# Optimization experiments

Measured on AMD Instinct MI355X. Metric: run time of the kernel, lower is better.

The kernel has to match this reference:

```python
import jax, jax.numpy as jnp
import numpy as np

# LIF params (from norse LIFParameters in __init__)
DT = 0.001
TAU_SYN_INV = 100.0   # 1/0.01
TAU_MEM_INV = 50.0    # 1/0.02
V_TH = 0.5
V_LEAK = 0.0
V_RESET = 0.0
ALPHA = 100.0         # superspike surrogate slope
# STDP params (additive, hardbound=False)
A_PRE = 0.001
A_POST = 0.001
TAU_PRE_INV = 0.5
TAU_POST_INV = 0.5
ETA_PLUS = 0.01
ETA_MINUS = 0.0001

T_STEPS, BATCH, IN_DIM, HID, N_LBL = 50, 256, 1024, 4096, 10

@jax.custom_vjp
def spike(x):
    return (x >= 0).astype(x.dtype)

def _spike_fwd(x):
    return (x >= 0).astype(x.dtype), x

def _spike_bwd(res, g):
    # norse 'super' (SuperSpike) surrogate gradient
    return (g / (ALPHA * jnp.abs(res) + 1.0) ** 2,)

spike.defvjp(_spike_fwd, _spike_bwd)


def setup_inputs() -> dict:
    key = jax.random.key(0)
    k1, k2, k3, k4 = jax.random.split(key, 4)
    x = (jax.random.uniform(k1, (T_STEPS, BATCH, IN_DIM)) < 0.1).astype(jnp.float32)
    label = jax.random.randint(k2, (BATCH,), 0, N_LBL)
    # positive weights inside the STDP bound [0, 0.3]
    w_in0 = jax.random.uniform(k3, (HID, IN_DIM), dtype=jnp.float32) * 0.3
    w_rec0 = jax.random.uniform(k4, (HID, HID), dtype=jnp.float32) * 0.05
    return {"x": x, "label": label, "w_in0": w_in0, "w_rec0": w_rec0, "num_labels": N_LBL}


def reference(x, label, w_in0, w_rec0, num_labels):
    T, B, I = x.shape
    H = w_in0.shape[0]
    f32 = x.dtype
    # fixed block assignments (init_assignments)
    npd = H // num_labels
    assignments = jnp.clip(jnp.arange(H) // npd, 0, num_labels - 1)
    a = jax.nn.one_hot(assignments, num_labels, dtype=f32)       # (H, L)
    b = jnp.clip(a.sum(axis=0), 1.0, None)                        # (L,)

    def step(carry, pre):
        v, i, z, w_in, w_rec, tp_i, tq_i, tp_r, tq_r, sc = carry
        # --- LIF recurrent cell (norse lif_step semantics) ---
        in_cur = pre @ w_in.T + z @ w_rec.T                       # (B, H)
        v_dec = v + DT * TAU_MEM_INV * ((V_LEAK - v) + i)
        i_dec = i - DT * TAU_SYN_INV * i
        z_new = spike(v_dec - V_TH)
        v_new = (1.0 - z_new) * v_dec + z_new * V_RESET
        i_new = i_dec + in_cur
        # --- STDP on input weights (additive, no hardbound) ---
        tp_i = tp_i + DT * TAU_PRE_INV * (-tp_i + A_PRE * pre)    # (B, I) pre trace
        tq_i = tq_i + DT * TAU_POST_INV * (-tq_i + A_POST * z_new)  # (B, H) post trace
        w_in = (w_in
                + ETA_PLUS * jnp.einsum('bh,bi->hi', z_new, tp_i)
                - ETA_MINUS * jnp.einsum('bh,bi->hi', tq_i, pre))
        # --- STDP on recurrent weights; pre spikes = previous outputs (z) ---
        tp_r = tp_r + DT * TAU_PRE_INV * (-tp_r + A_PRE * z)
        tq_r = tq_r + DT * TAU_POST_INV * (-tq_r + A_POST * z_new)
        w_rec = (w_rec
                 + ETA_PLUS * jnp.einsum('bh,bj->hj', z_new, tp_r)
                 - ETA_MINUS * jnp.einsum('bh,bj->hj', tq_r, z))
        sc = sc + z_new
        return (v_new, i_new, z_new, w_in, w_rec, tp_i, tq_i, tp_r, tq_r, sc), z_new.sum()

    carry0 = (jnp.zeros((B, H), f32), jnp.zeros((B, H), f32), jnp.zeros((B, H), f32),
              w_in0, w_rec0,
              jnp.zeros((B, I), f32), jnp.zeros((B, H), f32),
              jnp.zeros((B, H), f32), jnp.zeros((B, H), f32),
              jnp.zeros((B, H), f32))
    carry, per_t = jax.lax.scan(step, carry0, x)
    _, _, _, w_in_f, w_rec_f, _, _, _, _, sc = carry
    logits = (sc @ a) / (T * b)                                   # (B, L)
    total_spikes = per_t.sum()
    spike_count = jax.ops.segment_sum(sc, label, num_segments=num_labels)  # (L, H)
    label_count = T * jax.ops.segment_sum(jnp.ones((B,), f32), label, num_segments=num_labels)
    return logits, total_spikes, w_in_f, w_rec_f, spike_count, label_count
```

## Files before the change

### kernel.cpp

```cpp
#include <hip/hip_runtime.h>

typedef unsigned short u16;
typedef unsigned char u8;
typedef unsigned int u32;
typedef long i64;
typedef __attribute__((ext_vector_type(4))) float f32x4;
typedef __attribute__((ext_vector_type(4))) int i32x4;
typedef __attribute__((ext_vector_type(4))) u16 u16x4;

#define TSTEPS 50
#define BB 256
#define II 1024
#define HH 4096
#define LL 10
#define NPLANE ((size_t)BB*HH)
#define HB ((size_t)HH*BB)
#define IB ((size_t)II*BB)
#define TC 10
#define NSLOT 11
#define QSCALE 5.0e6f
#define WSCALE 64.0f

__device__ __forceinline__ u16 f2bf(float f){
  u32 u = __float_as_uint(f);
  u += 0x7fffu + ((u >> 16) & 1u);
  return (u16)(u >> 16);
}
__device__ __forceinline__ float bf2f(u16 u){ return __uint_as_float(((u32)u) << 16); }
__device__ __forceinline__ int wrapslot(int s){ return s >= NSLOT ? s - NSLOT : s; }

__device__ __forceinline__ u8 f2fp8(float v){
  if (v < 0.0009765625f) return 0;
  if (v < 0.015625f) return (u8)__float2int_rn(v * 512.f);
  u32 b = __float_as_uint(v);
  b += 0x7ffffu + ((b >> 20) & 1u);
  int e = (int)((b >> 23) & 255) - 120;
  u32 m = (b >> 20) & 7u;
  return (u8)((e << 3) | m);
}

__device__ __forceinline__ void async_cp16(const void* g, void* l){
  auto gp = (const __attribute__((address_space(1))) void*)(unsigned long long)(g);
  auto lp = (__attribute__((address_space(3))) void*)(unsigned int)(unsigned long long)(l);
  __builtin_amdgcn_global_load_lds(gp, lp, 16, 0, 0);
}

__global__ void __launch_bounds__(256) gemm_fwd(
    const u8* __restrict__ xbt, const u8* __restrict__ wib,
    const u8* __restrict__ zb,  const u8* __restrict__ wrb,
    u16* __restrict__ pbuf)
{
  __shared__ u8 lsA[2][64*64];
  __shared__ u8 lsB[2][128*64];
  const int tid = threadIdx.x, lane = tid & 63, wid = tid >> 6;
  const int wm = wid & 1, wn = wid >> 1;

  int bid = blockIdx.x;
  int oid = (bid & 7)*80 + (bid >> 3);
  int z   = oid >> 7;
  int rem = oid & 127;
  int n0  = (rem >> 2) * 128;
  int m0  = (rem & 3) * 64;

  const u8* __restrict__ Ab; const u8* __restrict__ Bb;
  int lda, ldb, kbase;
  if (z == 0){ Ab = xbt; lda = II; Bb = wib; ldb = II; kbase = 0; }
  else       { Ab = zb;  lda = HH; Bb = wrb; ldb = HH; kbase = (z-1)*1024; }
  u16* __restrict__ C = pbuf + (size_t)z*NPLANE;

  const int lrow = lane >> 2;
  const int lcb  = (lane & 3) << 4;

  auto STAGE = [&](int buf, int k0){
    int kg = kbase + k0;
    {
      int q = wid;
      int row = q*16 + lrow;
      int cb = lcb ^ (((row >> 1) & 3) << 4);
      async_cp16(Ab + (size_t)(m0 + row)*lda + kg + cb, (char*)lsA[buf] + q*1024);
    }
#pragma unroll
    for (int c = 0; c < 2; ++c){
      int q = c*4 + wid;
      int row = q*16 + lrow;
      int cb = lcb ^ (((row >> 1) & 3) << 4);
      async_cp16(Bb + (size_t)(n0 + row)*ldb + kg + cb, (char*)lsB[buf] + q*1024);
    }
  };

  f32x4 acc[2][4];
#pragma unroll
  for (int a=0;a<2;++a)
#pragma unroll
    for (int b=0;b<4;++b) acc[a][b] = f32x4{0.f,0.f,0.f,0.f};

  const int g16 = lane >> 4;
  STAGE(0, 0);
#pragma unroll 1
  for (int kt = 0; kt < 16; ++kt){
    int cur = kt & 1;
    if (kt < 15){
      STAGE(cur ^ 1, (kt+1)*64);
      asm volatile("s_waitcnt vmcnt(3)" ::: "memory");
    } else {
      asm volatile("s_waitcnt vmcnt(0)" ::: "memory");
    }
    __builtin_amdgcn_s_barrier();
#pragma unroll
    for (int kk = 0; kk < 2; ++kk){
      int unit = kk*2 + (g16 >> 1);
      int lo8  = (g16 & 1) << 3;
      i64 af[2], bfr[4];
#pragma unroll
      for (int fm=0; fm<2; ++fm){
        int ra = wm*32 + fm*16 + (lane & 15);
        af[fm] = *(const i64*)((const char*)lsA[cur] + ra*64 +
                               (((unit ^ ((ra >> 1) & 3)) << 4) + lo8));
      }
#pragma unroll
      for (int fn=0; fn<4; ++fn){
        int rb = wn*64 + fn*16 + (lane & 15);
        bfr[fn] = *(const i64*)((const char*)lsB[cur] + rb*64 +
                                (((unit ^ ((rb >> 1) & 3)) << 4) + lo8));
      }
#pragma unroll
      for (int fm=0; fm<2; ++fm)
#pragma unroll
        for (int fn=0; fn<4; ++fn)
          acc[fm][fn] = __builtin_amdgcn_mfma_f32_16x16x32_fp8_fp8(af[fm], bfr[fn], acc[fm][fn], 0, 0, 0);
    }
    __builtin_amdgcn_s_barrier();
  }

#pragma unroll
  for (int fm=0; fm<2; ++fm)
#pragma unroll
    for (int fn=0; fn<4; ++fn)
#pragma unroll
      for (int r=0; r<4; ++r){
        int row = m0 + wm*32 + fm*16 + ((lane >> 4) << 2) + r;
        int col = n0 + wn*64 + fn*16 + (lane & 15);
        C[(size_t)row*HH + col] = f2bf(acc[fm][fn][r]);
      }
}

__global__ void __launch_bounds__(512) gemm_chunk(
    const u8* __restrict__ zRing, const u8* __restrict__ uRing,
    const u8* __restrict__ tpi01s,
    int s0, int first, float* __restrict__ o_wrec, float* __restrict__ o_win)
{
  __shared__ u8 lsA[2][256*64];
  __shared__ u8 lsB[2][256*64];
  const int tid = threadIdx.x, lane = tid & 63, wid = tid >> 6;
  const int xcd = blockIdx.x & 7;
  const int local = blockIdx.x >> 3;
  const int g16 = lane >> 4;
  const int lrow = lane >> 2;
  const int lcb  = (lane & 3) << 4;

  if (local < 32){
    const int wm = wid & 1, wn = wid >> 1;
    int tm = (xcd >> 1)*4 + (local & 3);
    int tn = (xcd & 1)*8 + (local >> 2);
    int m0 = tm*256, n0 = tn*256;

    int offA[2], offB[2], ldso[2];
#pragma unroll
    for (int c=0;c<2;++c){
      int q = c*8 + wid;
      int row = q*16 + lrow;
      int cb = lcb ^ (((row >> 1) & 3) << 4);
      offA[c] = (m0 + row)*BB + cb;
      offB[c] = (n0 + row)*BB + cb;
      ldso[c] = q*1024;
    }

    auto STAGE = [&](int buf, int idx){
      int j  = idx >> 2;
      int k0 = (idx & 3) << 6;
      int sA = wrapslot(s0 + j + 1);
      int sB = wrapslot(s0 + j);
      const u8* __restrict__ Aslab = zRing + (size_t)sA*HB;
      const u8* __restrict__ Bslab = uRing + (size_t)sB*HB;
#pragma unroll
      for (int c=0;c<2;++c){
        async_cp16(Aslab + offA[c] + k0, (char*)lsA[buf] + ldso[c]);
        async_cp16(Bslab + offB[c] + k0, (char*)lsB[buf] + ldso[c]);
      }
    };

    i32x4 acc[8][4];
#pragma unroll
    for (int a=0;a<8;++a)
#pragma unroll
      for (int b=0;b<4;++b) acc[a][b] = i32x4{0,0,0,0};

    STAGE(0, 0);
#pragma unroll 1
    for (int idx = 0; idx < 4*TC; ++idx){
      int cur = idx & 1;
      if (idx < 4*TC-1){
        STAGE(cur ^ 1, idx+1);
        asm volatile("s_waitcnt vmcnt(4)" ::: "memory");
      } else {
        asm volatile("s_waitcnt vmcnt(0)" ::: "memory");
      }
      __builtin_amdgcn_s_barrier();
      __builtin_amdgcn_s_setprio(1);
      i32x4 bfr[4];
#pragma unroll
      for (int fn=0; fn<4; ++fn){
        int rb = wn*64 + fn*16 + (lane & 15);
        bfr[fn] = *(const i32x4*)((const char*)lsB[cur] + rb*64 + ((g16 ^ ((rb >> 1) & 3)) << 4));
      }
#pragma unroll
      for (int fm=0; fm<8; ++fm){
        int ra = wm*128 + fm*16 + (lane & 15);
        i32x4 af = *(const i32x4*)((const char*)lsA[cur] + ra*64 + ((g16 ^ ((ra >> 1) & 3)) << 4));
#pragma unroll
        for (int fn=0; fn<4; ++fn)
          acc[fm][fn] = __builtin_amdgcn_mfma_i32_16x16x64_i8(af, bfr[fn], acc[fm][fn], 0, 0, 0);
      }
      __builtin_amdgcn_s_setprio(0);
      __builtin_amdgcn_s_barrier();
    }

#pragma unroll
    for (int fm=0; fm<8; ++fm)
#pragma unroll
      for (int fn=0; fn<4; ++fn)
#pragma unroll
        for (int r=0; r<4; ++r){
          int row = m0 + wm*128 + fm*16 + ((lane >> 4) << 2) + r;
          int col = n0 + wn*64 + fn*16 + (lane & 15);
          size_t cidx = (size_t)row*HH + col;
          if (first) o_wrec[cidx] = (float)acc[fm][fn][r];
          else       o_wrec[cidx] += (float)acc[fm][fn][r];
        }
  } else {
    const int wm = wid & 1, wn = wid >> 1;
    int l2 = local - 32;
    int tm = (xcd >> 1)*8 + (l2 & 7);
    int tn = (xcd & 1)*4 + (l2 >> 3);
    int m0 = tm*128, n0 = tn*128;

    int offA, offB, ldso;
    {
      int q = wid;
      int row = q*16 + lrow;
      int cb = lcb ^ (((row >> 1) & 3) << 4);
      offA = (m0 + row)*BB + cb;
      offB = (n0 + row)*BB + cb;
      ldso = q*1024;
    }

    auto STAGE = [&](int buf, int idx){
      int j  = idx >> 2;
      int k0 = (idx & 3) << 6;
      int sA = wrapslot(s0 + j + 1);
      const u8* __restrict__ Aslab = zRing + (size_t)sA*HB;
      const u8* __restrict__ Bslab = tpi01s + (size_t)sA*IB;
      async_cp16(Aslab + offA + k0, (char*)lsA[buf] + ldso);
      async_cp16(Bslab + offB + k0, (char*)lsB[buf] + ldso);
    };

    i32x4 acc[4][2];
#pragma unroll
    for (int a=0;a<4;++a)
#pragma unroll
      for (int b=0;b<2;++b) acc[a][b] = i32x4{0,0,0,0};

    STAGE(0, 0);
#pragma unroll 1
    for (int idx = 0; idx < 4*TC; ++idx){
      int cur = idx & 1;
      if (idx < 4*TC-1){
        STAGE(cur ^ 1, idx+1);
        asm volatile("s_waitcnt vmcnt(2)" ::: "memory");
      } else {
        asm volatile("s_waitcnt vmcnt(0)" ::: "memory");
      }
      __builtin_amdgcn_s_barrier();
      __builtin_amdgcn_s_setprio(1);
      i32x4 bfr[2];
#pragma unroll
      for (int fn=0; fn<2; ++fn){
        int rb = wn*32 + fn*16 + (lane & 15);
        bfr[fn] = *(const i32x4*)((const char*)lsB[cur] + rb*64 + ((g16 ^ ((rb >> 1) & 3)) << 4));
      }
#pragma unroll
      for (int fm=0; fm<4; ++fm){
        int ra = wm*64 + fm*16 + (lane & 15);
        i32x4 af = *(const i32x4*)((const char*)lsA[cur] + ra*64 + ((g16 ^ ((ra >> 1) & 3)) << 4));
#pragma unroll
        for (int fn=0; fn<2; ++fn)
          acc[fm][fn] = __builtin_amdgcn_mfma_i32_16x16x64_i8(af, bfr[fn], acc[fm][fn], 0, 0, 0);
      }
      __builtin_amdgcn_s_setprio(0);
      __builtin_amdgcn_s_barrier();
    }

#pragma unroll
    for (int fm=0; fm<4; ++fm)
#pragma unroll
      for (int fn=0; fn<2; ++fn)
#pragma unroll
        for (int r=0; r<4; ++r){
          int row = m0 + wm*64 + fm*16 + ((lane >> 4) << 2) + r;
          int col = n0 + wn*32 + fn*16 + (lane & 15);
          size_t cidx = (size_t)row*II + col;
          if (first) o_win[cidx] = (float)acc[fm][fn][r];
          else       o_win[cidx] += (float)acc[fm][fn][r];
        }
  }
}

__device__ __forceinline__ void prep_body(
    const float* __restrict__ x, int t, int i0, int b0, int tid,
    u8* __restrict__ xb_buf, float* __restrict__ tpi,
    u8* __restrict__ tpi01s, int slot,
    u8* ls)
{
  u8 vp[4];
#pragma unroll
  for (int e=0;e<4;++e){
    int f = e*256 + tid;
    int il = f & 63, bl = f >> 6;
    size_t ix = ((size_t)t*BB + b0+bl)*II + i0 + il;
    size_t is = (size_t)(b0+bl)*II + i0 + il;
    float xv = x[ix];
    xb_buf[is] = (xv != 0.f) ? 0x38 : 0;
    float p = tpi[is]; p += 0.0005f*(0.001f*xv - p); tpi[is] = p;
    vp[e] = (u8)__float2int_rn(p * QSCALE);
  }
#pragma unroll
  for (int e=0;e<4;++e){
    int f=e*256+tid; int il=f&63, bl=f>>6;
    ls[il*17+bl] = vp[e];
  }
  __syncthreads();
#pragma unroll
  for (int e=0;e<4;++e){
    int f=e*256+tid; int bl=f&15, il=f>>4;
    size_t oi = (size_t)slot*IB + (size_t)(i0+il)*BB + b0 + bl;
    tpi01s[oi] = ls[il*17+bl];
  }
}

__global__ void __launch_bounds__(256) prep0(
    const float* __restrict__ x, u8* __restrict__ xb_buf,
    float* __restrict__ tpi, u8* __restrict__ tpi01s)
{
  __shared__ u8 ls[64*17];
  int bid = blockIdx.x;
  prep_body(x, 0, (bid & 15)*64, (bid >> 4)*16, threadIdx.x,
            xb_buf, tpi, tpi01s, 1, ls);
}

__global__ void __launch_bounds__(256) step_state(
    const u16* __restrict__ pbuf,
    float* __restrict__ v, float* __restrict__ iS, float* __restrict__ sc,
    float* __restrict__ u,
    u8* __restrict__ zb, u8* __restrict__ zRing, u8* __restrict__ uRing,
    int slotZ,
    const float* __restrict__ x, int tnext, int do_prep,
    u8* __restrict__ xb_buf, float* __restrict__ tpi,
    u8* __restrict__ tpi01s, int slotP)
{
  __shared__ u8 ls[2][64*17];
  const int tid = threadIdx.x;
  const int bid = blockIdx.x;

  if (bid < 1024){
    const int h0 = (bid & 63) * 64;
    const int b0 = (bid >> 6) * 16;
    u8 vz[4], vu[4];
#pragma unroll
    for (int e=0;e<4;++e){
      int f = e*256 + tid;
      int hl = f & 63, bl = f >> 6;
      size_t idx = (size_t)(b0+bl)*HH + h0 + hl;
      float ic = (bf2f(pbuf[idx]) + bf2f(pbuf[idx + NPLANE]) + bf2f(pbuf[idx + 2*NPLANE])
               +  bf2f(pbuf[idx + 3*NPLANE]) + bf2f(pbuf[idx + 4*NPLANE])) * (1.0f/WSCALE);
      float vv = v[idx], ii = iS[idx];
      float vdec = vv + 0.05f*((0.0f - vv) + ii);
      float idec = ii - 0.1f*ii;
      float z = (vdec >= 0.5f) ? 1.0f : 0.0f;
      v[idx] = (vdec >= 0.5f) ? 0.0f : vdec;
      iS[idx] = idec + ic;
      float uu = u[idx]; uu += 0.0005f*(0.001f*z - uu); u[idx] = uu;
      sc[idx] += z;
      zb[idx] = (vdec >= 0.5f) ? 0x38 : 0;
      vz[e] = (vdec >= 0.5f) ? 1 : 0;
      vu[e] = (u8)__float2int_rn(uu * QSCALE);
    }
#pragma unroll
    for (int e=0;e<4;++e){
      int f=e*256+tid; int hl=f&63, bl=f>>6; int o = hl*17+bl;
      ls[0][o]=vz[e]; ls[1][o]=vu[e];
    }
    __syncthreads();
#pragma unroll
    for (int e=0;e<4;++e){
      int f=e*256+tid; int bl=f&15, hl=f>>4; int o=hl*17+bl;
      size_t oi = (size_t)slotZ*HB + (size_t)(h0+hl)*BB + b0 + bl;
      zRing[oi]=ls[0][o]; uRing[oi]=ls[1][o];
    }
  } else {
    if (!do_prep) return;
    int r = bid - 1024;
    prep_body(x, tnext, (r & 15)*64, (r >> 4)*16, tid,
              xb_buf, tpi, tpi01s, slotP, ls[0]);
  }
}

__global__ void __launch_bounds__(256) cast_fp8(const f32x4* __restrict__ w0,
                                                u32* __restrict__ wb, long long n4){
  long long i = (long long)blockIdx.x*blockDim.x + threadIdx.x;
  long long stride = (long long)gridDim.x*blockDim.x;
  for (; i < n4; i += stride){
    f32x4 vv = w0[i];
    u32 o = (u32)f2fp8(vv[0]*WSCALE)
          | ((u32)f2fp8(vv[1]*WSCALE) << 8)
          | ((u32)f2fp8(vv[2]*WSCALE) << 16)
          | ((u32)f2fp8(vv[3]*WSCALE) << 24);
    wb[i] = o;
  }
}

__global__ void __launch_bounds__(256) fin_w(const f32x4* __restrict__ w0,
                                             f32x4* __restrict__ acc,
                                             float scale, long long n4){
  long long i = (long long)blockIdx.x*blockDim.x + threadIdx.x;
  long long stride = (long long)gridDim.x*blockDim.x;
  for (; i < n4; i += stride){
    f32x4 a = acc[i], w = w0[i];
#pragma unroll
    for (int j=0;j<4;++j) a[j] = w[j] + scale*a[j];
    acc[i] = a;
  }
}

__global__ void __launch_bounds__(256) fin_logits(const float* __restrict__ sc,
                                                  float* __restrict__ logits, float* __restrict__ total){
  __shared__ float bins[LL];
  const int tid = threadIdx.x;
  const int b = blockIdx.x;
  if (tid < LL) bins[tid] = 0.f;
  __syncthreads();
#pragma unroll
  for (int e=0;e<16;++e){
    int h = e*256 + tid;
    float vv = sc[(size_t)b*HH + h];
    int a = h/409; if (a > 9) a = 9;
    atomicAdd(&bins[a], vv);
  }
  __syncthreads();
  if (tid < LL){
    float cnt = (tid==9) ? 415.f : 409.f;
    logits[b*LL + tid] = bins[tid] / (50.f * cnt);
  }
  if (tid == 0){
    float s = 0.f;
    for (int l=0;l<LL;++l) s += bins[l];
    atomicAdd(total, s);
  }
}

__global__ void __launch_bounds__(256) fin_spikecnt(const float* __restrict__ sc,
                                                    const int* __restrict__ label, float* __restrict__ out){
  int h = blockIdx.x*256 + threadIdx.x;
  int bs = blockIdx.y*32;
  float acc[LL];
#pragma unroll
  for (int j=0;j<LL;++j) acc[j] = 0.f;
  for (int b=bs; b<bs+32; ++b){
    int l = label[b];
    float vv = sc[(size_t)b*HH + h];
#pragma unroll
    for (int j=0;j<LL;++j) acc[j] += (j==l) ? vv : 0.f;
  }
#pragma unroll
  for (int j=0;j<LL;++j)
    if (acc[j] != 0.f) atomicAdd(&out[(size_t)j*HH + h], acc[j]);
}

__global__ void __launch_bounds__(256) fin_labelcnt(const int* __restrict__ label, float* __restrict__ out){
  __shared__ int bins[LL];
  const int tid = threadIdx.x;
  if (tid < LL) bins[tid] = 0;
  __syncthreads();
  atomicAdd(&bins[label[tid]], 1);
  __syncthreads();
  if (tid < LL) out[tid] = 50.f * (float)bins[tid];
}

extern "C" void kernel_launch(void* const* d_in, const int* in_sizes, int n_in,
                              void* d_out, int out_size, void* d_ws, size_t ws_size,
                              hipStream_t stream)
{
  (void)in_sizes; (void)n_in; (void)out_size; (void)ws_size;
  const float* x      = (const float*)d_in[0];
  const int*   label  = (const int*)d_in[1];
  const float* w_in0  = (const float*)d_in[2];
  const float* w_rec0 = (const float*)d_in[3];

  float* out      = (float*)d_out;
  float* o_logits = out;
  float* o_total  = out + 2560;
  float* o_win    = out + 2561;
  float* o_wrec   = o_win + (size_t)HH*II;
  float* o_sc     = o_wrec + (size_t)HH*HH;
  float* o_lc     = o_sc + (size_t)LL*HH;

  char* cur = (char*)d_ws;
  auto alloc = [&](size_t bytes)->char*{ char* p = cur; cur += (bytes + 255) & ~(size_t)255; return p; };
  u8*    wib    = (u8*)   alloc((size_t)HH*II);
  u8*    wrb    = (u8*)   alloc((size_t)HH*HH);
  float* v      = (float*)alloc(NPLANE*4);
  float* iS     = (float*)alloc(NPLANE*4);
  float* sc     = (float*)alloc(NPLANE*4);
  float* u      = (float*)alloc(NPLANE*4);
  u16*   pbuf   = (u16*)  alloc(5*NPLANE*2);
  u8*    zb     = (u8*)   alloc(NPLANE);
  u8*    xb_buf = (u8*)   alloc((size_t)BB*II);
  float* tpi    = (float*)alloc((size_t)BB*II*4);
  u8*    zRing  = (u8*)   alloc((size_t)NSLOT*HB);
  u8*    uRing  = (u8*)   alloc((size_t)NSLOT*HB);
  u8*    tpi01s = (u8*)   alloc((size_t)NSLOT*IB);

  hipMemsetAsync(v,     0, NPLANE*4, stream);
  hipMemsetAsync(iS,    0, NPLANE*4, stream);
  hipMemsetAsync(sc,    0, NPLANE*4, stream);
  hipMemsetAsync(u,     0, NPLANE*4, stream);
  hipMemsetAsync(zb,    0, NPLANE, stream);
  hipMemsetAsync(tpi,   0, (size_t)BB*II*4, stream);
  hipMemsetAsync(zRing, 0, HB, stream);
  hipMemsetAsync(uRing, 0, HB, stream);
  hipMemsetAsync(o_total, 0, 4, stream);
  hipMemsetAsync(o_sc,  0, (size_t)LL*HH*4, stream);

  cast_fp8<<<1024, 256, 0, stream>>>((const f32x4*)w_in0,  (u32*)wib, (long long)HH*II/4);
  cast_fp8<<<2048, 256, 0, stream>>>((const f32x4*)w_rec0, (u32*)wrb, (long long)HH*HH/4);
  prep0<<<256, 256, 0, stream>>>(x, xb_buf, tpi, tpi01s);

  for (int t = 0; t < TSTEPS; ++t){
    gemm_fwd<<<640, 256, 0, stream>>>(xb_buf, wib, zb, wrb, pbuf);

    step_state<<<1280, 256, 0, stream>>>(
        pbuf, v, iS, sc, u, zb, zRing, uRing, (t+1) % NSLOT,
        x, t+1, (t < TSTEPS-1) ? 1 : 0,
        xb_buf, tpi, tpi01s, (t+2) % NSLOT);

    if ((t+1) % TC == 0){
      int s0 = (t+1-TC) % NSLOT;
      gemm_chunk<<<512, 512, 0, stream>>>(zRing, uRing, tpi01s,
                                          s0, (t+1 == TC) ? 1 : 0,
                                          o_wrec, o_win);
    }
  }

  fin_w<<<2048, 256, 0, stream>>>((const f32x4*)w_rec0, (f32x4*)o_wrec, 0.01f/QSCALE, (long long)HH*HH/4);
  fin_w<<<1024, 256, 0, stream>>>((const f32x4*)w_in0,  (f32x4*)o_win,  0.01f/QSCALE, (long long)HH*II/4);

  fin_logits  <<<BB, 256, 0, stream>>>(sc, o_logits, o_total);
  fin_spikecnt<<<dim3(HH/256, 8), 256, 0, stream>>>(sc, label, o_sc);
  fin_labelcnt<<<1, 256, 0, stream>>>(label, o_lc);
}
```

Measured before the change: 1.761 ms.

## Enlarge STDP chunk, fuse final weight update, shrink spike-count and trace storage

The STDP outer-product chunk grows from 10 to 25 timesteps, so gemm_chunk runs twice instead of five times and the fp32 output weights are read and rewritten fewer times. The final w0 + scale*acc step is folded into the last gemm_chunk epilogue, which removes the separate fin_w passes. The per-neuron spike count drops to u8 and the post trace u to bf16, cutting per-step state traffic in step_state. The costs are ring buffers with 26 slots (more workspace memory) and lower precision on the u trace, which may slightly change the quantized uRing values.

```diff
diff --git a/kernel.cpp b/kernel.cpp
--- a/kernel.cpp
+++ b/kernel.cpp
@@ -6,7 +6,6 @@
 typedef long i64;
 typedef __attribute__((ext_vector_type(4))) float f32x4;
 typedef __attribute__((ext_vector_type(4))) int i32x4;
-typedef __attribute__((ext_vector_type(4))) u16 u16x4;
 
 #define TSTEPS 50
 #define BB 256
@@ -16,8 +15,8 @@
 #define NPLANE ((size_t)BB*HH)
 #define HB ((size_t)HH*BB)
 #define IB ((size_t)II*BB)
-#define TC 10
-#define NSLOT 11
+#define TC 25
+#define NSLOT 26
 #define QSCALE 5.0e6f
 #define WSCALE 64.0f
 
@@ -147,7 +146,10 @@
 __global__ void __launch_bounds__(512) gemm_chunk(
     const u8* __restrict__ zRing, const u8* __restrict__ uRing,
     const u8* __restrict__ tpi01s,
-    int s0, int first, float* __restrict__ o_wrec, float* __restrict__ o_win)
+    int s0, int first, int lastd,
+    float* __restrict__ o_wrec, float* __restrict__ o_win,
+    const float* __restrict__ w0rec, const float* __restrict__ w0in,
+    float scale)
 {
   __shared__ u8 lsA[2][256*64];
   __shared__ u8 lsB[2][256*64];
@@ -234,8 +236,9 @@
           int row = m0 + wm*128 + fm*16 + ((lane >> 4) << 2) + r;
           int col = n0 + wn*64 + fn*16 + (lane & 15);
           size_t cidx = (size_t)row*HH + col;
-          if (first) o_wrec[cidx] = (float)acc[fm][fn][r];
-          else       o_wrec[cidx] += (float)acc[fm][fn][r];
+          float a = (float)acc[fm][fn][r];
+          if (!first) a += o_wrec[cidx];
+          o_wrec[cidx] = lastd ? (w0rec[cidx] + scale*a) : a;
         }
   } else {
     const int wm = wid & 1, wn = wid >> 1;
@@ -309,8 +312,9 @@
           int row = m0 + wm*64 + fm*16 + ((lane >> 4) << 2) + r;
           int col = n0 + wn*32 + fn*16 + (lane & 15);
           size_t cidx = (size_t)row*II + col;
-          if (first) o_win[cidx] = (float)acc[fm][fn][r];
-          else       o_win[cidx] += (float)acc[fm][fn][r];
+          float a = (float)acc[fm][fn][r];
+          if (!first) a += o_win[cidx];
+          o_win[cidx] = lastd ? (w0in[cidx] + scale*a) : a;
         }
   }
 }
@@ -359,8 +363,8 @@
 
 __global__ void __launch_bounds__(256) step_state(
     const u16* __restrict__ pbuf,
-    float* __restrict__ v, float* __restrict__ iS, float* __restrict__ sc,
-    float* __restrict__ u,
+    float* __restrict__ v, float* __restrict__ iS, u8* __restrict__ sc,
+    u16* __restrict__ u,
     u8* __restrict__ zb, u8* __restrict__ zRing, u8* __restrict__ uRing,
     int slotZ,
     const float* __restrict__ x, int tnext, int do_prep,
@@ -385,13 +389,14 @@
       float vv = v[idx], ii = iS[idx];
       float vdec = vv + 0.05f*((0.0f - vv) + ii);
       float idec = ii - 0.1f*ii;
-      float z = (vdec >= 0.5f) ? 1.0f : 0.0f;
-      v[idx] = (vdec >= 0.5f) ? 0.0f : vdec;
+      bool spk = (vdec >= 0.5f);
+      float z = spk ? 1.0f : 0.0f;
+      v[idx] = spk ? 0.0f : vdec;
       iS[idx] = idec + ic;
-      float uu = u[idx]; uu += 0.0005f*(0.001f*z - uu); u[idx] = uu;
-      sc[idx] += z;
-      zb[idx] = (vdec >= 0.5f) ? 0x38 : 0;
-      vz[e] = (vdec >= 0.5f) ? 1 : 0;
+      float uu = bf2f(u[idx]); uu += 0.0005f*(0.001f*z - uu); u[idx] = f2bf(uu);
+      sc[idx] = (u8)(sc[idx] + (spk ? 1 : 0));
+      zb[idx] = spk ? 0x38 : 0;
+      vz[e] = spk ? 1 : 0;
       vu[e] = (u8)__float2int_rn(uu * QSCALE);
     }
 #pragma unroll
@@ -428,20 +433,7 @@
   }
 }
 
-__global__ void __launch_bounds__(256) fin_w(const f32x4* __restrict__ w0,
-                                             f32x4* __restrict__ acc,
-                                             float scale, long long n4){
-  long long i = (long long)blockIdx.x*blockDim.x + threadIdx.x;
-  long long stride = (long long)gridDim.x*blockDim.x;
-  for (; i < n4; i += stride){
-    f32x4 a = acc[i], w = w0[i];
-#pragma unroll
-    for (int j=0;j<4;++j) a[j] = w[j] + scale*a[j];
-    acc[i] = a;
-  }
-}
-
-__global__ void __launch_bounds__(256) fin_logits(const float* __restrict__ sc,
+__global__ void __launch_bounds__(256) fin_logits(const u8* __restrict__ sc,
                                                   float* __restrict__ logits, float* __restrict__ total){
   __shared__ float bins[LL];
   const int tid = threadIdx.x;
@@ -451,7 +443,7 @@
 #pragma unroll
   for (int e=0;e<16;++e){
     int h = e*256 + tid;
-    float vv = sc[(size_t)b*HH + h];
+    float vv = (float)sc[(size_t)b*HH + h];
     int a = h/409; if (a > 9) a = 9;
     atomicAdd(&bins[a], vv);
   }
@@ -467,7 +459,7 @@
   }
 }
 
-__global__ void __launch_bounds__(256) fin_spikecnt(const float* __restrict__ sc,
+__global__ void __launch_bounds__(256) fin_spikecnt(const u8* __restrict__ sc,
                                                     const int* __restrict__ label, float* __restrict__ out){
   int h = blockIdx.x*256 + threadIdx.x;
   int bs = blockIdx.y*32;
@@ -476,7 +468,7 @@
   for (int j=0;j<LL;++j) acc[j] = 0.f;
   for (int b=bs; b<bs+32; ++b){
     int l = label[b];
-    float vv = sc[(size_t)b*HH + h];
+    float vv = (float)sc[(size_t)b*HH + h];
 #pragma unroll
     for (int j=0;j<LL;++j) acc[j] += (j==l) ? vv : 0.f;
   }
@@ -519,8 +511,8 @@
   u8*    wrb    = (u8*)   alloc((size_t)HH*HH);
   float* v      = (float*)alloc(NPLANE*4);
   float* iS     = (float*)alloc(NPLANE*4);
-  float* sc     = (float*)alloc(NPLANE*4);
-  float* u      = (float*)alloc(NPLANE*4);
+  u8*    sc     = (u8*)   alloc(NPLANE);
+  u16*   u      = (u16*)  alloc(NPLANE*2);
   u16*   pbuf   = (u16*)  alloc(5*NPLANE*2);
   u8*    zb     = (u8*)   alloc(NPLANE);
   u8*    xb_buf = (u8*)   alloc((size_t)BB*II);
@@ -531,8 +523,8 @@
 
   hipMemsetAsync(v,     0, NPLANE*4, stream);
   hipMemsetAsync(iS,    0, NPLANE*4, stream);
-  hipMemsetAsync(sc,    0, NPLANE*4, stream);
-  hipMemsetAsync(u,     0, NPLANE*4, stream);
+  hipMemsetAsync(sc,    0, NPLANE, stream);
+  hipMemsetAsync(u,     0, NPLANE*2, stream);
   hipMemsetAsync(zb,    0, NPLANE, stream);
   hipMemsetAsync(tpi,   0, (size_t)BB*II*4, stream);
   hipMemsetAsync(zRing, 0, HB, stream);
@@ -556,12 +548,11 @@
       int s0 = (t+1-TC) % NSLOT;
       gemm_chunk<<<512, 512, 0, stream>>>(zRing, uRing, tpi01s,
                                           s0, (t+1 == TC) ? 1 : 0,
-                                          o_wrec, o_win);
-    }
-  }
-
-  fin_w<<<2048, 256, 0, stream>>>((const f32x4*)w_rec0, (f32x4*)o_wrec, 0.01f/QSCALE, (long long)HH*HH/4);
-  fin_w<<<1024, 256, 0, stream>>>((const f32x4*)w_in0,  (f32x4*)o_win,  0.01f/QSCALE, (long long)HH*II/4);
+                                          (t+1 == TSTEPS) ? 1 : 0,
+                                          o_wrec, o_win, w_rec0, w_in0,
+                                          0.01f/QSCALE);
+    }
+  }
 
   fin_logits  <<<BB, 256, 0, stream>>>(sc, o_logits, o_total);
   fin_spikecnt<<<dim3(HH/256, 8), 256, 0, stream>>>(sc, label, o_sc);
```

Result: faster. 1.588 ms (-9.8%).
